# Performance work log

Hardware: AMD Instinct MI355X
Metric: run time of the kernel (lower is better)

The kernel has to match this reference:

```python
import jax, jax.numpy as jnp
import numpy as np

EPS = 1e-5


def spline_conv(x, src, dst, pseudo, W, root, bias, num_nodes, K=5):
    """Degree-1 open B-spline conv (torch_spline_conv semantics), mean aggregation.
    W: [kernel_total, Cin, Cout]. kernel_total==1 means trivial basis (kernel_size=1)."""
    E = src.shape[0]
    Cin = x.shape[1]
    KT = W.shape[0]
    x_j = x[src]                                            # [E, Cin] edge gather
    deg = jax.ops.segment_sum(jnp.ones((E,), x.dtype), dst, num_segments=num_nodes)
    deg = jnp.maximum(deg, 1.0)
    if KT == 1:
        agg = jax.ops.segment_sum(x_j, dst, num_segments=num_nodes)
        out = (agg / deg[:, None]) @ W[0]
    else:
        v = pseudo * (K - 1)                                # open spline: v in [0, K-1]
        f = jnp.clip(jnp.floor(v), 0.0, K - 2)
        frac = v - f                                        # [E, 2]
        fi = f.astype(jnp.int32)
        # bucket basis-weighted source features by (kernel_index, dst) then one dense einsum
        h = jnp.zeros((KT * num_nodes, Cin), x.dtype)
        for s0 in (0, 1):
            for s1 in (0, 1):
                b0 = frac[:, 0] if s0 else 1.0 - frac[:, 0]
                b1 = frac[:, 1] if s1 else 1.0 - frac[:, 1]
                basis = b0 * b1                             # [E]
                wi = (fi[:, 0] + s0) + K * (fi[:, 1] + s1)  # [E] kernel index in [0,25)
                seg = wi * num_nodes + dst
                h = h + jax.ops.segment_sum(basis[:, None] * x_j, seg,
                                            num_segments=KT * num_nodes)
        agg = jnp.einsum('knc,kco->no', h.reshape(KT, num_nodes, Cin), W)
        out = agg / deg[:, None]
    return out + x @ root + bias


def batch_norm(x, gamma, beta):
    m = x.mean(axis=0)
    var = jnp.mean((x - m) ** 2, axis=0)
    return gamma * (x - m) * jax.lax.rsqrt(var + EPS) + beta


def setup_inputs() -> dict:
    key = jax.random.key(0)
    ks = jax.random.split(key, 8)
    N, E, Cin, Cout = 50000, 800000, 32, 64
    x = jax.random.normal(ks[0], (N, Cin), jnp.float32)
    edge_index = jax.random.randint(ks[1], (2, E), 0, N, jnp.int32)
    edge_attr = jax.random.uniform(ks[2], (E, 2), jnp.float32)
    s = 0.1
    return {
        'x': x, 'edge_index': edge_index, 'edge_attr': edge_attr,
        'w1': jax.random.normal(ks[3], (25, Cin, Cout), jnp.float32) * s,
        'r1': jax.random.normal(ks[4], (Cin, Cout), jnp.float32) * s,
        'b1': jnp.zeros((Cout,), jnp.float32),
        'g1': jnp.ones((Cout,), jnp.float32),
        'beta1': jnp.zeros((Cout,), jnp.float32),
        'w2': jax.random.normal(ks[5], (25, Cout, Cout), jnp.float32) * s,
        'r2': jax.random.normal(ks[6], (Cout, Cout), jnp.float32) * s,
        'b2': jnp.zeros((Cout,), jnp.float32),
        'g2': jnp.ones((Cout,), jnp.float32),
        'beta2': jnp.zeros((Cout,), jnp.float32),
        'ws': jax.random.normal(ks[7], (1, Cin, Cout), jnp.float32) * s,
        'rs': jax.random.normal(jax.random.fold_in(key, 99), (Cin, Cout), jnp.float32) * s,
        'bs': jnp.zeros((Cout,), jnp.float32),
        'gs': jnp.ones((Cout,), jnp.float32),
        'betas': jnp.zeros((Cout,), jnp.float32),
    }


def reference(x, edge_index, edge_attr, w1, r1, b1, g1, beta1,
              w2, r2, b2, g2, beta2, ws, rs, bs, gs, betas):
    N = x.shape[0]
    src, dst = edge_index[0], edge_index[1]
    h = jax.nn.elu(batch_norm(spline_conv(x, src, dst, edge_attr, w1, r1, b1, N), g1, beta1))
    left = batch_norm(spline_conv(h, src, dst, edge_attr, w2, r2, b2, N), g2, beta2)
    short = batch_norm(spline_conv(x, src, dst, edge_attr, ws, rs, bs, N), gs, betas)
    return jax.nn.elu(left + short)
```

## Files before the change

kernel.cpp:

```cpp
#include <hip/hip_runtime.h>

#define NN 50000
#define NE 800000

typedef __attribute__((ext_vector_type(8))) short bf16x8;
typedef __attribute__((ext_vector_type(4))) float f32x4;
typedef __attribute__((ext_vector_type(2))) float f32x2;

__device__ __forceinline__ unsigned short f2bf(float f) {
    union { float f; unsigned u; } v; v.f = f;
    unsigned r = v.u + 0x7FFFu + ((v.u >> 16) & 1u);
    return (unsigned short)(r >> 16);
}

__device__ __forceinline__ int4 ld_ep(const int4* ep, unsigned idx) {
    return *(const int4*)((const char*)ep + (size_t)(idx * 16u));
}
__device__ __forceinline__ unsigned ld_xu(const unsigned* X, unsigned byteoff) {
    return *(const unsigned*)((const char*)X + (size_t)byteoff);
}

__device__ __forceinline__ f32x2 unpack2(unsigned u) {
    union { unsigned u; float f; } a, b;
    a.u = u << 16;
    b.u = u & 0xFFFF0000u;
    return f32x2{a.f, b.f};
}

__device__ __forceinline__ f32x2 pk_mul_hib(f32x2 w, f32x2 x) {
    f32x2 d;
    asm("v_pk_mul_f32 %0, %1, %2 op_sel:[1,0] op_sel_hi:[1,1]"
        : "=v"(d) : "v"(w), "v"(x));
    return d;
}
__device__ __forceinline__ void pk_fma_lob(f32x2& h, f32x2 w, f32x2 t) {
    asm("v_pk_fma_f32 %0, %1, %2, %0 op_sel:[0,0,0] op_sel_hi:[0,1,1]"
        : "+v"(h) : "v"(w), "v"(t));
}

__device__ __forceinline__ int us_idx(int kk, int r, int m) {
    return kk*544 + (r >> 3)*136 + m*8 + (r & 7);
}

template<bool HS>
__device__ __forceinline__ void edge_acc2(f32x2* h, f32x2& hs, const int4& p, f32x2 x) {
    const f32x2 zero = {0.f, 0.f};
    f32x2 vp = {__int_as_float(p.z), __int_as_float(p.w)};
    f32x2 wxy[5];
#pragma unroll
    for (int r = 0; r < 5; ++r) {
        f32x2 wr = 1.f - __builtin_elementwise_abs(vp - (float)r);
        wxy[r] = __builtin_elementwise_max(wr, zero);
    }
    if (HS) hs += x;
#pragma unroll
    for (int r1 = 0; r1 < 5; ++r1) {
        f32x2 ty = pk_mul_hib(wxy[r1], x);
#pragma unroll
        for (int r0 = 0; r0 < 5; ++r0)
            pk_fma_lob(h[r1*5 + r0], wxy[r0], ty);
    }
}

__device__ __forceinline__ float eh_reduce(f32x2 v, int eh, int stride) {
    float mine  = eh ? v.y : v.x;
    float other = eh ? v.x : v.y;
    return mine + __shfl_xor(other, stride);
}

__global__ __launch_bounds__(256) void k_zero(int* degi, int* cur, float* stats) {
    int i = blockIdx.x*256 + threadIdx.x;
    int stride = gridDim.x*256;
    for (int j = i; j < NN; j += stride) { degi[j] = 0; cur[j] = 0; }
    if (i < 384) stats[i] = 0.f;
}

__global__ __launch_bounds__(256) void k_hist(const int* __restrict__ dst, int* degi) {
    int e = blockIdx.x*256 + threadIdx.x;
    if (e < NE) atomicAdd(&degi[dst[e]], 1);
}

__global__ __launch_bounds__(256) void k_scan_block(const int* __restrict__ degi,
                                                    int* off, int* bsum) {
    __shared__ int sh[256];
    int t = threadIdx.x;
    int base = blockIdx.x * 1024;
    int v[4]; int s = 0;
#pragma unroll
    for (int j = 0; j < 4; j++) {
        int idx = base + t*4 + j;
        v[j] = (idx < NN) ? degi[idx] : 0;
        s += v[j];
    }
    sh[t] = s; __syncthreads();
    for (int ofs = 1; ofs < 256; ofs <<= 1) {
        int x = (t >= ofs) ? sh[t - ofs] : 0;
        __syncthreads();
        sh[t] += x;
        __syncthreads();
    }
    int ex = sh[t] - s;
#pragma unroll
    for (int j = 0; j < 4; j++) {
        int idx = base + t*4 + j;
        if (idx < NN) off[idx] = ex;
        ex += v[j];
    }
    if (t == 255) bsum[blockIdx.x] = sh[255];
}

__global__ __launch_bounds__(256) void k_scan_top(const int* __restrict__ bsum,
                                                  int* bpre, int nb) {
    __shared__ int sh[256];
    int t = threadIdx.x;
    int s = (t < nb) ? bsum[t] : 0;
    sh[t] = s; __syncthreads();
    for (int ofs = 1; ofs < 256; ofs <<= 1) {
        int x = (t >= ofs) ? sh[t - ofs] : 0;
        __syncthreads();
        sh[t] += x;
        __syncthreads();
    }
    if (t < nb) bpre[t] = sh[t] - s;
}

__global__ __launch_bounds__(256) void k_scan_add(int* off, const int* __restrict__ bpre) {
    int i = blockIdx.x*256 + threadIdx.x;
    if (i < NN) off[i] += bpre[i >> 10];
    if (i == 0) off[NN] = NE;
}

__global__ __launch_bounds__(256) void k_scatter(const int* __restrict__ src,
                                                 const int* __restrict__ dst,
                                                 const float* __restrict__ ea,
                                                 const int* __restrict__ off, int* cur,
                                                 int4* __restrict__ ep) {
    int e = blockIdx.x*256 + threadIdx.x;
    if (e >= NE) return;
    int d = dst[e];
    int p = off[d] + atomicAdd(&cur[d], 1);
    float v0 = ea[2*e]     * 4.f;
    float v1 = ea[2*e + 1] * 4.f;
    ep[p] = make_int4(src[e], 0, __float_as_int(v0), __float_as_int(v1));
}

__global__ __launch_bounds__(256) void k_xbf(const float* __restrict__ x,
                                             unsigned short* __restrict__ xb) {
    int i = blockIdx.x*256 + threadIdx.x;
    if (i >= NN*8) return;
    float4 v = ((const float4*)x)[i];
    uint2 pk;
    pk.x = (unsigned)f2bf(v.x) | ((unsigned)f2bf(v.y) << 16);
    pk.y = (unsigned)f2bf(v.z) | ((unsigned)f2bf(v.w) << 16);
    ((uint2*)xb)[i] = pk;
}

__global__ __launch_bounds__(256) void k_wprep(const float* __restrict__ W,
                                               const float* __restrict__ root,
                                               int KTC, unsigned short* Wb) {
    int tid = blockIdx.x*256 + threadIdx.x;
    int lane = tid & 63, cot = (tid >> 6) & 3, kk = tid >> 8;
    int co = 16*cot + (lane & 15);
    int kbase = kk*32 + ((lane >> 4) * 8);
    union { unsigned short s[8]; uint4 v; } u;
#pragma unroll
    for (int j = 0; j < 8; j++) {
        int k = kbase + j;
        float val = (k < KTC) ? W[(size_t)k*64 + co] : root[(size_t)(k - KTC)*64 + co];
        u.s[j] = f2bf(val);
    }
    *(uint4*)(Wb + (size_t)tid * 8) = u.v;
}

__global__ __launch_bounds__(512, 4) void k_conv1s(
        const unsigned* __restrict__ Xbf,
        const int* __restrict__ off,
        const int4* __restrict__ ep,
        const unsigned short* __restrict__ Wb1,
        const unsigned short* __restrict__ WbS,
        const float* __restrict__ b1,
        const float* __restrict__ bs,
        float* __restrict__ agg1,
        float* __restrict__ aggS) {
    __shared__ __align__(16) unsigned short hb[28*544];
    const int t = threadIdx.x;
    const int g = t >> 5;
    const int q = t & 31;
    const int chp = q & 15;
    const int eh = q >> 4;
    const int n0 = blockIdx.x * 16;
    const int n = n0 + g;

    f32x2 h[25], hs = {0.f, 0.f};
#pragma unroll
    for (int i = 0; i < 25; ++i) h[i] = f32x2{0.f, 0.f};

    const int ebeg = off[n], eend = off[n + 1];
    const int last = eend - 1;
    const float rdeg = 1.f / (float)max(eend - ebeg, 1);

    for (int i = ebeg; i < eend; i += 8) {
        int4 p[4]; unsigned u[4];
#pragma unroll
        for (int uu = 0; uu < 4; ++uu)
            p[uu] = ld_ep(ep, (unsigned)min(i + 2*uu + eh, last));
#pragma unroll
        for (int uu = 0; uu < 4; ++uu) {
            u[uu] = ld_xu(Xbf, (unsigned)p[uu].x * 64u + (unsigned)chp * 4u);
            if (i + 2*uu + eh > last) u[uu] = 0u;
        }
#pragma unroll
        for (int uu = 0; uu < 4; ++uu)
            edge_acc2<true>(h, hs, p[uu], unpack2(u[uu]));
    }

    const int c = 2*chp + eh;
    const int bw = us_idx(0, c, g);
#pragma unroll
    for (int wi = 0; wi < 25; ++wi)
        hb[wi*544 + bw] = f2bf(eh_reduce(h[wi], eh, 16) * rdeg);
    hb[26*544 + bw] = f2bf(eh_reduce(hs, eh, 16) * rdeg);
    {
        unsigned ux = Xbf[(unsigned)n * 16u + (unsigned)chp];
        unsigned short xb = eh ? (unsigned short)(ux >> 16)
                               : (unsigned short)(ux & 0xFFFFu);
        hb[25*544 + bw] = xb;
        hb[27*544 + bw] = xb;
    }
    __syncthreads();

    const int lane = t & 63, w = t >> 6;
    const int m = lane & 15, qq = lane >> 4;
    const int co = (w & 3)*16 + m;
    if (w < 4) {
        f32x4 acc = {0.f, 0.f, 0.f, 0.f};
        for (int kk = 0; kk < 26; ++kk) {
            bf16x8 av = *(const bf16x8*)&hb[kk*544 + qq*136 + m*8];
            bf16x8 bv = *(const bf16x8*)(Wb1 + (size_t)((kk*4 + w)*64 + lane) * 8);
            acc = __builtin_amdgcn_mfma_f32_16x16x32_bf16(av, bv, acc, 0, 0, 0);
        }
        const float bb = b1[co];
#pragma unroll
        for (int r = 0; r < 4; ++r)
            agg1[(size_t)(n0 + qq*4 + r)*64 + co] = acc[r] + bb;
    } else {
        f32x4 accs = {0.f, 0.f, 0.f, 0.f};
#pragma unroll
        for (int s = 0; s < 2; ++s) {
            bf16x8 av = *(const bf16x8*)&hb[(26 + s)*544 + qq*136 + m*8];
            bf16x8 bv = *(const bf16x8*)(WbS + (size_t)((s*4 + (w & 3))*64 + lane) * 8);
            accs = __builtin_amdgcn_mfma_f32_16x16x32_bf16(av, bv, accs, 0, 0, 0);
        }
        const float bb = bs[co];
#pragma unroll
        for (int r = 0; r < 4; ++r)
            aggS[(size_t)(n0 + qq*4 + r)*64 + co] = accs[r] + bb;
    }
}

__global__ __launch_bounds__(512, 4) void k_conv2(
        const unsigned* __restrict__ Xbf,
        const int* __restrict__ off,
        const int4* __restrict__ ep,
        const unsigned short* __restrict__ Wb2,
        const float* __restrict__ b2,
        float* __restrict__ agg) {
    __shared__ __align__(16) unsigned short hb[52*544];
    const int t = threadIdx.x, lane = t & 63, w = t >> 6;
    const int n0 = blockIdx.x * 16;
    const int chp = lane & 31, eh = lane >> 5;
    const int c = 2*chp + eh;
    const int kh = c >> 5, r = c & 31;

#pragma unroll
    for (int nn = 0; nn < 2; ++nn) {
        const int g = 2*w + nn;
        const int n = n0 + g;
        f32x2 h[25]; f32x2 hsd = {0.f, 0.f};
#pragma unroll
        for (int i = 0; i < 25; ++i) h[i] = f32x2{0.f, 0.f};

        const int ebeg = off[n], eend = off[n + 1];
        const int last = eend - 1;
        const float rdeg = 1.f / (float)max(eend - ebeg, 1);

        for (int i = ebeg; i < eend; i += 8) {
            int4 p[4]; unsigned u[4];
#pragma unroll
            for (int uu = 0; uu < 4; ++uu)
                p[uu] = ld_ep(ep, (unsigned)min(i + 2*uu + eh, last));
#pragma unroll
            for (int uu = 0; uu < 4; ++uu) {
                u[uu] = ld_xu(Xbf, (unsigned)p[uu].x * 128u + (unsigned)chp * 4u);
                if (i + 2*uu + eh > last) u[uu] = 0u;
            }
#pragma unroll
            for (int uu = 0; uu < 4; ++uu)
                edge_acc2<false>(h, hsd, p[uu], unpack2(u[uu]));
        }

        const int bw = us_idx(0, r, g);
#pragma unroll
        for (int wi = 0; wi < 25; ++wi)
            hb[(wi*2 + kh)*544 + bw] = f2bf(eh_reduce(h[wi], eh, 32) * rdeg);
        {
            unsigned ux = Xbf[(unsigned)n * 32u + (unsigned)chp];
            hb[(50 + kh)*544 + bw] =
                (unsigned short)(eh ? (ux >> 16) : (ux & 0xFFFFu));
        }
    }
    __syncthreads();

    if (w >= 4) return;

    const int m = lane & 15, qq = lane >> 4;
    f32x4 acc = {0.f, 0.f, 0.f, 0.f};
    for (int kk = 0; kk < 52; ++kk) {
        bf16x8 av = *(const bf16x8*)&hb[kk*544 + qq*136 + m*8];
        bf16x8 bv = *(const bf16x8*)(Wb2 + (size_t)((kk*4 + w)*64 + lane) * 8);
        acc = __builtin_amdgcn_mfma_f32_16x16x32_bf16(av, bv, acc, 0, 0, 0);
    }
    const int co = w*16 + m;
    const float bb = b2[co];
#pragma unroll
    for (int rr = 0; rr < 4; ++rr)
        agg[(size_t)(n0 + qq*4 + rr)*64 + co] = acc[rr] + bb;
}

__global__ __launch_bounds__(256) void k_bnstats(const float* __restrict__ agg, float* stats) {
    __shared__ float sh0[256], sh1[256];
    int t = threadIdx.x;
    float s = 0.f, ss = 0.f;
    int stride = gridDim.x * 256;
    for (int i = blockIdx.x*256 + t; i < NN*64; i += stride) {
        float v = agg[i];
        s += v; ss += v*v;
    }
    sh0[t] = s; sh1[t] = ss;
    __syncthreads();
    if (t < 64) {
        float a = sh0[t] + sh0[t+64] + sh0[t+128] + sh0[t+192];
        float b = sh1[t] + sh1[t+64] + sh1[t+128] + sh1[t+192];
        atomicAdd(&stats[t], a);
        atomicAdd(&stats[64 + t], b);
    }
}

__device__ __forceinline__ float eluf(float u) { return u > 0.f ? u : expm1f(u); }

__global__ __launch_bounds__(256) void k_bn_elu(const float* __restrict__ agg,
                                                const float* __restrict__ stats,
                                                const float* __restrict__ gamma,
                                                const float* __restrict__ beta,
                                                unsigned short* __restrict__ outb) {
    int i = blockIdx.x*256 + threadIdx.x;
    if (i >= NN*16) return;
    float4 v = ((const float4*)agg)[i];
    float r[4] = {v.x, v.y, v.z, v.w};
    int c0 = (i << 2) & 63;
#pragma unroll
    for (int j = 0; j < 4; j++) {
        int c = c0 + j;
        float mu = stats[c] * (1.f/NN);
        float var = stats[64 + c] * (1.f/NN) - mu*mu;
        float sc = gamma[c] * rsqrtf(fmaxf(var, 0.f) + 1e-5f);
        r[j] = eluf((r[j] - mu)*sc + beta[c]);
    }
    uint2 pk;
    pk.x = (unsigned)f2bf(r[0]) | ((unsigned)f2bf(r[1]) << 16);
    pk.y = (unsigned)f2bf(r[2]) | ((unsigned)f2bf(r[3]) << 16);
    ((uint2*)outb)[i] = pk;
}

__global__ __launch_bounds__(256) void k_bn_final(const float* __restrict__ a2,
                                                  const float* __restrict__ st2,
                                                  const float* __restrict__ g2,
                                                  const float* __restrict__ be2,
                                                  const float* __restrict__ as,
                                                  const float* __restrict__ sts,
                                                  const float* __restrict__ gs,
                                                  const float* __restrict__ bes,
                                                  float* __restrict__ out) {
    int i = blockIdx.x*256 + threadIdx.x;
    if (i >= NN*16) return;
    float4 v2 = ((const float4*)a2)[i];
    float4 vs = ((const float4*)as)[i];
    float r2v[4] = {v2.x, v2.y, v2.z, v2.w};
    float rsv[4] = {vs.x, vs.y, vs.z, vs.w};
    float o[4];
    int c0 = (i << 2) & 63;
#pragma unroll
    for (int j = 0; j < 4; j++) {
        int c = c0 + j;
        float mu2 = st2[c] * (1.f/NN);
        float var2 = st2[64 + c] * (1.f/NN) - mu2*mu2;
        float sc2 = g2[c] * rsqrtf(fmaxf(var2, 0.f) + 1e-5f);
        float mus = sts[c] * (1.f/NN);
        float vars = sts[64 + c] * (1.f/NN) - mus*mus;
        float scs = gs[c] * rsqrtf(fmaxf(vars, 0.f) + 1e-5f);
        float u = (r2v[j] - mu2)*sc2 + be2[c] + (rsv[j] - mus)*scs + bes[c];
        o[j] = eluf(u);
    }
    ((float4*)out)[i] = make_float4(o[0], o[1], o[2], o[3]);
}

extern "C" void kernel_launch(void* const* d_in, const int* in_sizes, int n_in,
                              void* d_out, int out_size, void* d_ws, size_t ws_size,
                              hipStream_t stream) {
    const float* x   = (const float*)d_in[0];
    const int*   ei  = (const int*)d_in[1];
    const float* ea  = (const float*)d_in[2];
    const float* w1  = (const float*)d_in[3];
    const float* r1  = (const float*)d_in[4];
    const float* b1  = (const float*)d_in[5];
    const float* g1  = (const float*)d_in[6];
    const float* be1 = (const float*)d_in[7];
    const float* w2  = (const float*)d_in[8];
    const float* r2  = (const float*)d_in[9];
    const float* b2  = (const float*)d_in[10];
    const float* g2  = (const float*)d_in[11];
    const float* be2 = (const float*)d_in[12];
    const float* wsN = (const float*)d_in[13];
    const float* rs  = (const float*)d_in[14];
    const float* bs  = (const float*)d_in[15];
    const float* gs  = (const float*)d_in[16];
    const float* bes = (const float*)d_in[17];
    const int* srcp = ei;
    const int* dstp = ei + NE;

    char* wsb = (char*)d_ws;
    size_t o = 0;
    auto alloc = [&](size_t bytes) -> char* {
        char* p = wsb + o;
        o += (bytes + 255) & ~(size_t)255;
        return p;
    };
    int*    degi    = (int*)   alloc((size_t)NN * 4);
    int*    cur     = (int*)   alloc((size_t)NN * 4);
    int*    off     = (int*)   alloc((size_t)(NN + 1) * 4);
    int*    bsum    = (int*)   alloc(256 * 4);
    int*    bpre    = (int*)   alloc(256 * 4);
    int4*   ep      = (int4*)  alloc((size_t)NE * 16);
    unsigned short* Wb1 = (unsigned short*)alloc(26 * 4096);
    unsigned short* WbS = (unsigned short*)alloc(2 * 4096);
    unsigned short* Wb2 = (unsigned short*)alloc(52 * 4096);
    float*  agg1    = (float*) alloc((size_t)NN * 64 * 4);
    float*  aggS    = (float*) alloc((size_t)NN * 64 * 4);
    unsigned short* h1bf = (unsigned short*)alloc((size_t)NN * 64 * 2);
    unsigned short* xbf  = (unsigned short*)alloc((size_t)NN * 32 * 2);
    float*  stats   = (float*) alloc(384 * 4);
    (void)ws_size; (void)in_sizes; (void)n_in; (void)out_size;

    float* out = (float*)d_out;

    k_zero<<<196, 256, 0, stream>>>(degi, cur, stats);
    k_hist<<<3125, 256, 0, stream>>>(dstp, degi);
    k_scan_block<<<49, 256, 0, stream>>>(degi, off, bsum);
    k_scan_top<<<1, 256, 0, stream>>>(bsum, bpre, 49);
    k_scan_add<<<196, 256, 0, stream>>>(off, bpre);
    k_scatter<<<3125, 256, 0, stream>>>(srcp, dstp, ea, off, cur, ep);

    k_xbf<<<1563, 256, 0, stream>>>(x, xbf);
    k_wprep<<<26, 256, 0, stream>>>(w1, r1, 800, Wb1);
    k_wprep<<<2, 256, 0, stream>>>(wsN, rs, 32, WbS);
    k_wprep<<<52, 256, 0, stream>>>(w2, r2, 1600, Wb2);

    k_conv1s<<<3125, 512, 0, stream>>>((const unsigned*)xbf, off, ep, Wb1, WbS,
                                       b1, bs, agg1, aggS);
    k_bnstats<<<256, 256, 0, stream>>>(agg1, stats);
    k_bn_elu<<<3125, 256, 0, stream>>>(agg1, stats, g1, be1, h1bf);

    k_conv2<<<3125, 512, 0, stream>>>((const unsigned*)h1bf, off, ep, Wb2, b2, agg1);
    k_bnstats<<<256, 256, 0, stream>>>(agg1, stats + 128);
    k_bnstats<<<256, 256, 0, stream>>>(aggS, stats + 256);
    k_bn_final<<<3125, 256, 0, stream>>>(agg1, stats + 128, g2, be2,
                                         aggS, stats + 256, gs, bes, out);
}
```

Before: 446.7 us.

## Sort nodes by degree and precompute bf16 spline basis weights per edge

Adds a counting sort of nodes by in-degree so each conv block processes nodes with similar edge counts, reducing wavefront divergence from uneven loop trip counts, and scatters results back through the permutation. The five per-axis B-spline basis weights are now computed once in the scatter kernel and stored as packed bf16 in a 32-byte edge record, removing the per-edge abs/max work from both conv kernels. The inner loop unroll drops from 4 to 2 edges per lane. The trade-offs are doubled edge-record bandwidth, bf16 rounding of the basis weights, extra setup kernels, and scattered output writes.

```diff
diff --git a/kernel.cpp b/kernel.cpp
--- a/kernel.cpp
+++ b/kernel.cpp
@@ -2,6 +2,7 @@
 
 #define NN 50000
 #define NE 800000
+#define DBINS 1024
 
 typedef __attribute__((ext_vector_type(8))) short bf16x8;
 typedef __attribute__((ext_vector_type(4))) float f32x4;
@@ -13,8 +14,8 @@
     return (unsigned short)(r >> 16);
 }
 
-__device__ __forceinline__ int4 ld_ep(const int4* ep, unsigned idx) {
-    return *(const int4*)((const char*)ep + (size_t)(idx * 16u));
+__device__ __forceinline__ int4 ld_ep2(const int4* ep, unsigned idx, int which) {
+    return *(const int4*)((const char*)ep + (size_t)(idx * 32u + (unsigned)which * 16u));
 }
 __device__ __forceinline__ unsigned ld_xu(const unsigned* X, unsigned byteoff) {
     return *(const unsigned*)((const char*)X + (size_t)byteoff);
@@ -43,15 +44,14 @@
 }
 
 template<bool HS>
-__device__ __forceinline__ void edge_acc2(f32x2* h, f32x2& hs, const int4& p, f32x2 x) {
-    const f32x2 zero = {0.f, 0.f};
-    f32x2 vp = {__int_as_float(p.z), __int_as_float(p.w)};
+__device__ __forceinline__ void edge_acc2(f32x2* h, f32x2& hs,
+                                          const int4& pa, const int4& pb, f32x2 x) {
     f32x2 wxy[5];
-#pragma unroll
-    for (int r = 0; r < 5; ++r) {
-        f32x2 wr = 1.f - __builtin_elementwise_abs(vp - (float)r);
-        wxy[r] = __builtin_elementwise_max(wr, zero);
-    }
+    wxy[0] = unpack2((unsigned)pa.y);
+    wxy[1] = unpack2((unsigned)pa.z);
+    wxy[2] = unpack2((unsigned)pa.w);
+    wxy[3] = unpack2((unsigned)pb.x);
+    wxy[4] = unpack2((unsigned)pb.y);
     if (HS) hs += x;
 #pragma unroll
     for (int r1 = 0; r1 < 5; ++r1) {
@@ -68,11 +68,13 @@
     return mine + __shfl_xor(other, stride);
 }
 
-__global__ __launch_bounds__(256) void k_zero(int* degi, int* cur, float* stats) {
+__global__ __launch_bounds__(256) void k_zero(int* degi, int* cur, float* stats,
+                                              int* dcnt, int* dcur) {
     int i = blockIdx.x*256 + threadIdx.x;
     int stride = gridDim.x*256;
     for (int j = i; j < NN; j += stride) { degi[j] = 0; cur[j] = 0; }
     if (i < 384) stats[i] = 0.f;
+    if (i < DBINS) { dcnt[i] = 0; dcur[i] = 0; }
 }
 
 __global__ __launch_bounds__(256) void k_hist(const int* __restrict__ dst, int* degi) {
@@ -130,6 +132,39 @@
     if (i == 0) off[NN] = NE;
 }
 
+__global__ __launch_bounds__(256) void k_dhist(const int* __restrict__ degi, int* dcnt) {
+    int n = blockIdx.x*256 + threadIdx.x;
+    if (n < NN) atomicAdd(&dcnt[min(degi[n], DBINS-1)], 1);
+}
+
+__global__ __launch_bounds__(256) void k_dscan(const int* __restrict__ dcnt, int* dbase) {
+    __shared__ int sh[256];
+    int t = threadIdx.x;
+    int v[4]; int s = 0;
+#pragma unroll
+    for (int j = 0; j < 4; j++) { v[j] = dcnt[t*4 + j]; s += v[j]; }
+    sh[t] = s; __syncthreads();
+    for (int ofs = 1; ofs < 256; ofs <<= 1) {
+        int x = (t >= ofs) ? sh[t - ofs] : 0;
+        __syncthreads();
+        sh[t] += x;
+        __syncthreads();
+    }
+    int ex = sh[t] - s;
+#pragma unroll
+    for (int j = 0; j < 4; j++) { dbase[t*4 + j] = ex; ex += v[j]; }
+}
+
+__global__ __launch_bounds__(256) void k_pscatter(const int* __restrict__ degi,
+                                                  const int* __restrict__ dbase,
+                                                  int* dcur, int* perm) {
+    int n = blockIdx.x*256 + threadIdx.x;
+    if (n >= NN) return;
+    int d = min(degi[n], DBINS-1);
+    int p = dbase[d] + atomicAdd(&dcur[d], 1);
+    perm[p] = n;
+}
+
 __global__ __launch_bounds__(256) void k_scatter(const int* __restrict__ src,
                                                  const int* __restrict__ dst,
                                                  const float* __restrict__ ea,
@@ -141,7 +176,15 @@
     int p = off[d] + atomicAdd(&cur[d], 1);
     float v0 = ea[2*e]     * 4.f;
     float v1 = ea[2*e + 1] * 4.f;
-    ep[p] = make_int4(src[e], 0, __float_as_int(v0), __float_as_int(v1));
+    unsigned w[5];
+#pragma unroll
+    for (int r = 0; r < 5; ++r) {
+        float wx = fmaxf(1.f - fabsf(v0 - (float)r), 0.f);
+        float wy = fmaxf(1.f - fabsf(v1 - (float)r), 0.f);
+        w[r] = (unsigned)f2bf(wx) | ((unsigned)f2bf(wy) << 16);
+    }
+    ep[2*p]     = make_int4(src[e], (int)w[0], (int)w[1], (int)w[2]);
+    ep[2*p + 1] = make_int4((int)w[3], (int)w[4], 0, 0);
 }
 
 __global__ __launch_bounds__(256) void k_xbf(const float* __restrict__ x,
@@ -176,6 +219,7 @@
         const unsigned* __restrict__ Xbf,
         const int* __restrict__ off,
         const int4* __restrict__ ep,
+        const int* __restrict__ perm,
         const unsigned short* __restrict__ Wb1,
         const unsigned short* __restrict__ WbS,
         const float* __restrict__ b1,
@@ -189,7 +233,7 @@
     const int chp = q & 15;
     const int eh = q >> 4;
     const int n0 = blockIdx.x * 16;
-    const int n = n0 + g;
+    const int n = perm[n0 + g];
 
     f32x2 h[25], hs = {0.f, 0.f};
 #pragma unroll
@@ -199,19 +243,17 @@
     const int last = eend - 1;
     const float rdeg = 1.f / (float)max(eend - ebeg, 1);
 
-    for (int i = ebeg; i < eend; i += 8) {
-        int4 p[4]; unsigned u[4];
-#pragma unroll
-        for (int uu = 0; uu < 4; ++uu)
-            p[uu] = ld_ep(ep, (unsigned)min(i + 2*uu + eh, last));
-#pragma unroll
-        for (int uu = 0; uu < 4; ++uu) {
-            u[uu] = ld_xu(Xbf, (unsigned)p[uu].x * 64u + (unsigned)chp * 4u);
-            if (i + 2*uu + eh > last) u[uu] = 0u;
-        }
-#pragma unroll
-        for (int uu = 0; uu < 4; ++uu)
-            edge_acc2<true>(h, hs, p[uu], unpack2(u[uu]));
+    for (int i = ebeg; i < eend; i += 4) {
+        const int e0 = i + eh, e1 = i + 2 + eh;
+        const unsigned i0 = (unsigned)min(e0, last), i1 = (unsigned)min(e1, last);
+        int4 a0 = ld_ep2(ep, i0, 0), b0 = ld_ep2(ep, i0, 1);
+        int4 a1 = ld_ep2(ep, i1, 0), b1 = ld_ep2(ep, i1, 1);
+        unsigned u0 = ld_xu(Xbf, (unsigned)a0.x * 64u + (unsigned)chp * 4u);
+        unsigned u1 = ld_xu(Xbf, (unsigned)a1.x * 64u + (unsigned)chp * 4u);
+        if (e0 > last) u0 = 0u;
+        if (e1 > last) u1 = 0u;
+        edge_acc2<true>(h, hs, a0, b0, unpack2(u0));
+        edge_acc2<true>(h, hs, a1, b1, unpack2(u1));
     }
 
     const int c = 2*chp + eh;
@@ -232,6 +274,8 @@
     const int lane = t & 63, w = t >> 6;
     const int m = lane & 15, qq = lane >> 4;
     const int co = (w & 3)*16 + m;
+    const int4 pn = ((const int4*)perm)[(n0 >> 2) + qq];
+    const int prow[4] = {pn.x, pn.y, pn.z, pn.w};
     if (w < 4) {
         f32x4 acc = {0.f, 0.f, 0.f, 0.f};
         for (int kk = 0; kk < 26; ++kk) {
@@ -242,7 +286,7 @@
         const float bb = b1[co];
 #pragma unroll
         for (int r = 0; r < 4; ++r)
-            agg1[(size_t)(n0 + qq*4 + r)*64 + co] = acc[r] + bb;
+            agg1[(size_t)prow[r]*64 + co] = acc[r] + bb;
     } else {
         f32x4 accs = {0.f, 0.f, 0.f, 0.f};
 #pragma unroll
@@ -254,7 +298,7 @@
         const float bb = bs[co];
 #pragma unroll
         for (int r = 0; r < 4; ++r)
-            aggS[(size_t)(n0 + qq*4 + r)*64 + co] = accs[r] + bb;
+            aggS[(size_t)prow[r]*64 + co] = accs[r] + bb;
     }
 }
 
@@ -262,6 +306,7 @@
         const unsigned* __restrict__ Xbf,
         const int* __restrict__ off,
         const int4* __restrict__ ep,
+        const int* __restrict__ perm,
         const unsigned short* __restrict__ Wb2,
         const float* __restrict__ b2,
         float* __restrict__ agg) {
@@ -275,7 +320,7 @@
 #pragma unroll
     for (int nn = 0; nn < 2; ++nn) {
         const int g = 2*w + nn;
-        const int n = n0 + g;
+        const int n = perm[n0 + g];
         f32x2 h[25]; f32x2 hsd = {0.f, 0.f};
 #pragma unroll
         for (int i = 0; i < 25; ++i) h[i] = f32x2{0.f, 0.f};
@@ -284,19 +329,17 @@
         const int last = eend - 1;
         const float rdeg = 1.f / (float)max(eend - ebeg, 1);
 
-        for (int i = ebeg; i < eend; i += 8) {
-            int4 p[4]; unsigned u[4];
-#pragma unroll
-            for (int uu = 0; uu < 4; ++uu)
-                p[uu] = ld_ep(ep, (unsigned)min(i + 2*uu + eh, last));
-#pragma unroll
-            for (int uu = 0; uu < 4; ++uu) {
-                u[uu] = ld_xu(Xbf, (unsigned)p[uu].x * 128u + (unsigned)chp * 4u);
-                if (i + 2*uu + eh > last) u[uu] = 0u;
-            }
-#pragma unroll
-            for (int uu = 0; uu < 4; ++uu)
-                edge_acc2<false>(h, hsd, p[uu], unpack2(u[uu]));
+        for (int i = ebeg; i < eend; i += 4) {
+            const int e0 = i + eh, e1 = i + 2 + eh;
+            const unsigned i0 = (unsigned)min(e0, last), i1 = (unsigned)min(e1, last);
+            int4 a0 = ld_ep2(ep, i0, 0), b0 = ld_ep2(ep, i0, 1);
+            int4 a1 = ld_ep2(ep, i1, 0), b1 = ld_ep2(ep, i1, 1);
+            unsigned u0 = ld_xu(Xbf, (unsigned)a0.x * 128u + (unsigned)chp * 4u);
+            unsigned u1 = ld_xu(Xbf, (unsigned)a1.x * 128u + (unsigned)chp * 4u);
+            if (e0 > last) u0 = 0u;
+            if (e1 > last) u1 = 0u;
+            edge_acc2<false>(h, hsd, a0, b0, unpack2(u0));
+            edge_acc2<false>(h, hsd, a1, b1, unpack2(u1));
         }
 
         const int bw = us_idx(0, r, g);
@@ -314,6 +357,8 @@
     if (w >= 4) return;
 
     const int m = lane & 15, qq = lane >> 4;
+    const int4 pn = ((const int4*)perm)[(n0 >> 2) + qq];
+    const int prow[4] = {pn.x, pn.y, pn.z, pn.w};
     f32x4 acc = {0.f, 0.f, 0.f, 0.f};
     for (int kk = 0; kk < 52; ++kk) {
         bf16x8 av = *(const bf16x8*)&hb[kk*544 + qq*136 + m*8];
@@ -324,7 +369,7 @@
     const float bb = b2[co];
 #pragma unroll
     for (int rr = 0; rr < 4; ++rr)
-        agg[(size_t)(n0 + qq*4 + rr)*64 + co] = acc[rr] + bb;
+        agg[(size_t)prow[rr]*64 + co] = acc[rr] + bb;
 }
 
 __global__ __launch_bounds__(256) void k_bnstats(const float* __restrict__ agg, float* stats) {
@@ -440,7 +485,11 @@
     int*    off     = (int*)   alloc((size_t)(NN + 1) * 4);
     int*    bsum    = (int*)   alloc(256 * 4);
     int*    bpre    = (int*)   alloc(256 * 4);
-    int4*   ep      = (int4*)  alloc((size_t)NE * 16);
+    int*    dcnt    = (int*)   alloc(DBINS * 4);
+    int*    dcur    = (int*)   alloc(DBINS * 4);
+    int*    dbase   = (int*)   alloc(DBINS * 4);
+    int*    perm    = (int*)   alloc((size_t)NN * 4);
+    int4*   ep      = (int4*)  alloc((size_t)NE * 32);
     unsigned short* Wb1 = (unsigned short*)alloc(26 * 4096);
     unsigned short* WbS = (unsigned short*)alloc(2 * 4096);
     unsigned short* Wb2 = (unsigned short*)alloc(52 * 4096);
@@ -453,11 +502,14 @@
 
     float* out = (float*)d_out;
 
-    k_zero<<<196, 256, 0, stream>>>(degi, cur, stats);
+    k_zero<<<196, 256, 0, stream>>>(degi, cur, stats, dcnt, dcur);
     k_hist<<<3125, 256, 0, stream>>>(dstp, degi);
     k_scan_block<<<49, 256, 0, stream>>>(degi, off, bsum);
     k_scan_top<<<1, 256, 0, stream>>>(bsum, bpre, 49);
     k_scan_add<<<196, 256, 0, stream>>>(off, bpre);
+    k_dhist<<<196, 256, 0, stream>>>(degi, dcnt);
+    k_dscan<<<1, 256, 0, stream>>>(dcnt, dbase);
+    k_pscatter<<<196, 256, 0, stream>>>(degi, dbase, dcur, perm);
     k_scatter<<<3125, 256, 0, stream>>>(srcp, dstp, ea, off, cur, ep);
 
     k_xbf<<<1563, 256, 0, stream>>>(x, xbf);
@@ -465,12 +517,12 @@
     k_wprep<<<2, 256, 0, stream>>>(wsN, rs, 32, WbS);
     k_wprep<<<52, 256, 0, stream>>>(w2, r2, 1600, Wb2);
 
-    k_conv1s<<<3125, 512, 0, stream>>>((const unsigned*)xbf, off, ep, Wb1, WbS,
+    k_conv1s<<<3125, 512, 0, stream>>>((const unsigned*)xbf, off, ep, perm, Wb1, WbS,
                                        b1, bs, agg1, aggS);
     k_bnstats<<<256, 256, 0, stream>>>(agg1, stats);
     k_bn_elu<<<3125, 256, 0, stream>>>(agg1, stats, g1, be1, h1bf);
 
-    k_conv2<<<3125, 512, 0, stream>>>((const unsigned*)h1bf, off, ep, Wb2, b2, agg1);
+    k_conv2<<<3125, 512, 0, stream>>>((const unsigned*)h1bf, off, ep, perm, Wb2, b2, agg1);
     k_bnstats<<<256, 256, 0, stream>>>(agg1, stats + 128);
     k_bnstats<<<256, 256, 0, stream>>>(aggS, stats + 256);
     k_bn_final<<<3125, 256, 0, stream>>>(agg1, stats + 128, g2, be2,
```

New measurement: 713.5 us. 1.6x slower.
